# Optimization experiments

Hardware: AMD Instinct MI355X
Metric: run time of the kernel (lower is better)

Reference implementation:

```python
import jax, jax.numpy as jnp
import numpy as np

NUM_EXPERTS = 8
AUX_LOSS_COEF = 0.01


def setup_inputs() -> dict:
    key = jax.random.key(0)
    ks = jax.random.split(key, 5)
    B, S, D, E, H = 4, 2048, 1024, NUM_EXPERTS, 4096
    scale = 0.02  # typical init scale so gelu/softmax stay in sane ranges
    return {
        "hidden_states": jax.random.normal(ks[0], (B, S, D), dtype=jnp.float32),
        "router_w": jax.random.normal(ks[1], (D, E), dtype=jnp.float32) * scale,
        "router_b": jnp.zeros((E,), dtype=jnp.float32),
        "w1": jax.random.normal(ks[2], (E, D, H), dtype=jnp.float32) * scale,
        "b1": jnp.zeros((E, H), dtype=jnp.float32),
        "w2": jax.random.normal(ks[3], (E, H, D), dtype=jnp.float32) * scale,
        "b2": jnp.zeros((E, D), dtype=jnp.float32),
    }


def reference(hidden_states, router_w, router_b, w1, b1, w2, b2):
    B, S, D = hidden_states.shape
    E = w1.shape[0]
    x = hidden_states.reshape(-1, D)  # [T, D] flattened tokens

    # Switch router: top-1 expert, combine weight = softmax prob of chosen expert
    logits = x @ router_w + router_b                      # [T, E]
    probs = jax.nn.softmax(logits, axis=-1)               # [T, E]
    sel = jnp.argmax(logits, axis=-1)                     # [T] int
    gate = jnp.take_along_axis(probs, sel[:, None], axis=1)[:, 0]  # [T]

    # Expert FFNs: per-expert Linear -> gelu -> Linear, masked top-1 combine.
    # Loop is over the small fixed expert count (structurally distinct weights).
    out = jnp.zeros_like(x)
    for e in range(E):
        h = jax.nn.gelu(x @ w1[e] + b1[e])                # [T, H]
        ye = h @ w2[e] + b2[e]                            # [T, D]
        mask = (sel == e).astype(x.dtype)
        out = out + (mask * gate)[:, None] * ye

    # Switch load-balancing auxiliary loss
    mean_probs = probs.mean(axis=0)                       # [E]
    assignments = jnp.mean(jax.nn.one_hot(sel, E, dtype=x.dtype), axis=0)  # [E]
    aux_loss = jnp.sum(mean_probs * assignments) * E
    total_loss = AUX_LOSS_COEF * aux_loss

    return out.reshape(B, S, D), total_loss
```

## Files before the change

### kernel.cpp

```cpp
#include <hip/hip_runtime.h>
#include <cstdint>

typedef __bf16 bf16_t;
typedef __attribute__((ext_vector_type(8))) __bf16 bf16x8;
typedef __attribute__((ext_vector_type(4))) float f32x4;
typedef unsigned short ushort_t;

#define TOKENS 8192
#define DIM 1024
#define HID 4096
#define NEXP 8


__device__ __forceinline__ void gl_lds16(const void* g, void* l) {
  __builtin_amdgcn_global_load_lds(
      (__attribute__((address_space(1))) void*)(void*)g,
      (__attribute__((address_space(3))) void*)l, 16, 0, 0);
}

__device__ __forceinline__ float gelu_fast(float x) {
  float x2 = x * x;
  float z2 = x * (1.59576912f + 0.07135482f * x2);
  float e = __expf(-z2);
  return x * __builtin_amdgcn_rcpf(1.f + e);
}

template <int N>
__device__ __forceinline__ void pwait() {
  __builtin_amdgcn_sched_barrier(0);
  if constexpr (N == 8) asm volatile("s_waitcnt vmcnt(8)" ::: "memory");
  else if constexpr (N == 6) asm volatile("s_waitcnt vmcnt(6)" ::: "memory");
  else asm volatile("s_waitcnt vmcnt(0)" ::: "memory");
  __builtin_amdgcn_sched_barrier(0);
  __builtin_amdgcn_s_barrier();
  __builtin_amdgcn_sched_barrier(0);
}
__device__ __forceinline__ void tbar() {
  __builtin_amdgcn_sched_barrier(0);
  __builtin_amdgcn_s_barrier();
  __builtin_amdgcn_sched_barrier(0);
}

__device__ __forceinline__ int xcd_chunk(int f, int nwg) {
  int q = nwg >> 3, r = nwg & 7;
  int xcd = f & 7, pos = f >> 3;
  return (xcd < r) ? (xcd * (q + 1) + pos) : (r * (q + 1) + (xcd - r) * q + pos);
}

__global__ void router_kernel(const float* __restrict__ x, const float* __restrict__ rw,
                              const float* __restrict__ rbias, bf16_t* __restrict__ xb,
                              int* __restrict__ sel, float* __restrict__ gate,
                              float* __restrict__ pprob, int* __restrict__ pcnt) {
  __shared__ float sprob[NEXP];
  __shared__ int scnt[NEXP];
  int t = threadIdx.x, lane = t & 63, wave = t >> 6;
  if (t < NEXP) { sprob[t] = 0.f; scnt[t] = 0; }
  __syncthreads();
  int tok = blockIdx.x * 4 + wave;
  const float* xp = x + (size_t)tok * DIM + lane * 16;
  float acc[NEXP];
#pragma unroll
  for (int e = 0; e < NEXP; ++e) acc[e] = 0.f;
  ushort_t xv[16];
#pragma unroll
  for (int j = 0; j < 16; j += 4) {
    float4 v = *(const float4*)(xp + j);
    const float* wr = rw + (size_t)(lane * 16 + j) * NEXP;
    float c[4] = {v.x, v.y, v.z, v.w};
#pragma unroll
    for (int d = 0; d < 4; ++d) {
      xv[j + d] = __builtin_bit_cast(ushort_t, (bf16_t)c[d]);
#pragma unroll
      for (int e = 0; e < NEXP; ++e) acc[e] += c[d] * wr[d * NEXP + e];
    }
  }
  {
    uint4* xop = (uint4*)(xb + (size_t)tok * DIM + lane * 16);
    xop[0] = ((uint4*)xv)[0];
    xop[1] = ((uint4*)xv)[1];
  }
#pragma unroll
  for (int s = 1; s < 64; s <<= 1)
#pragma unroll
    for (int e = 0; e < NEXP; ++e) acc[e] += __shfl_xor(acc[e], s);
  if (lane == 0) {
    float lg[NEXP];
#pragma unroll
    for (int e = 0; e < NEXP; ++e) lg[e] = acc[e] + rbias[e];
    float mx = lg[0]; int am = 0;
#pragma unroll
    for (int e = 1; e < NEXP; ++e) if (lg[e] > mx) { mx = lg[e]; am = e; }
    float p[NEXP]; float se = 0.f;
#pragma unroll
    for (int e = 0; e < NEXP; ++e) { p[e] = __expf(lg[e] - mx); se += p[e]; }
    float inv = 1.f / se;
#pragma unroll
    for (int e = 0; e < NEXP; ++e) { p[e] *= inv; atomicAdd(&sprob[e], p[e]); }
    sel[tok] = am;
    gate[tok] = p[am];
    atomicAdd(&scnt[am], 1);
  }
  __syncthreads();
  if (t < NEXP) {
    pprob[blockIdx.x * NEXP + t] = sprob[t];
    pcnt[blockIdx.x * NEXP + t] = scnt[t];
  }
}

__global__ void tcvt2_kernel(const float* __restrict__ w1, const float* __restrict__ w2,
                             bf16_t* __restrict__ w1t, bf16_t* __restrict__ w2t) {
  __shared__ float tile[64][65];
  int y = blockIdx.y;
  int which = y >> 3, e = y & 7;
  int R = which ? HID : DIM;
  int C = which ? DIM : HID;
  const float* src = (which ? w2 : w1) + (size_t)e * R * C;
  bf16_t* dst = (which ? w2t : w1t) + (size_t)e * R * C;
  int cbt = C >> 6;
  int rt = blockIdx.x / cbt, ct = blockIdx.x % cbt;
  int rb = rt * 64, cb = ct * 64;
  int t = threadIdx.x;
  int r = t >> 2, cq = (t & 3) * 16;
  const float* sp = src + (size_t)(rb + r) * C + cb + cq;
#pragma unroll
  for (int j = 0; j < 16; j += 4) {
    float4 v = *(const float4*)(sp + j);
    tile[r][cq + j + 0] = v.x; tile[r][cq + j + 1] = v.y;
    tile[r][cq + j + 2] = v.z; tile[r][cq + j + 3] = v.w;
  }
  __syncthreads();
  int oc = t >> 2, orr = (t & 3) * 16;
  ushort_t tmp[16];
#pragma unroll
  for (int j = 0; j < 16; ++j) {
    bf16_t b = (bf16_t)tile[orr + j][oc];
    tmp[j] = __builtin_bit_cast(ushort_t, b);
  }
  uint4* dp = (uint4*)(dst + (size_t)(cb + oc) * R + rb + orr);
  dp[0] = ((uint4*)tmp)[0];
  dp[1] = ((uint4*)tmp)[1];
}

__global__ void reduce_kernel(const float* __restrict__ pprob, const int* __restrict__ pcnt,
                              int nb, int* __restrict__ meta, float* __restrict__ loss_out) {
  __shared__ float fred[256];
  __shared__ int ired[256];
  int t = threadIdx.x;
  int e = t & 7, i0 = t >> 3;
  float fs = 0.f; int is = 0;
  for (int i = i0; i < nb; i += 32) { fs += pprob[i * 8 + e]; is += pcnt[i * 8 + e]; }
  fred[t] = fs; ired[t] = is;
  __syncthreads();
  if (t < NEXP) {
    float tp = 0.f; int tc = 0;
    for (int j = 0; j < 32; ++j) { tp += fred[j * 8 + t]; tc += ired[j * 8 + t]; }
    meta[t] = tc;
    fred[t] = tp;
    meta[16 + t] = 0;
  }
  __syncthreads();
  if (t == 0) {
    int off = 0; float loss = 0.f; int s1 = 0, s2 = 0;
    for (int q = 0; q < NEXP; ++q) {
      int c = meta[q];
      meta[8 + q] = off;
      int nt1 = (c + 255) >> 8;
      for (int m = 0; m < nt1; ++m) meta[32 + s1++] = (q << 16) | m;
      int nt2 = (c + 127) >> 7;
      for (int m = 0; m < nt2; ++m) meta[96 + s2++] = (q << 16) | m;
      off += c;
      loss += (fred[q] / (float)TOKENS) * ((float)c / (float)TOKENS);
    }
    meta[24] = s1;
    meta[25] = s2;
    *loss_out = loss * (float)NEXP * 0.01f;
  }
}

__global__ void scatter_kernel(const int* __restrict__ sel, int* __restrict__ meta,
                               int* __restrict__ idxl) {
  int tok = blockIdx.x * 256 + threadIdx.x;
  int lane = threadIdx.x & 63;
  int e = sel[tok];
  const int* offsets = meta + 8;
  int* cursors = meta + 16;
#pragma unroll
  for (int ex = 0; ex < NEXP; ++ex) {
    unsigned long long mask = __ballot(e == ex);
    if (e == ex) {
      int leader = __ffsll(mask) - 1;
      int total = __popcll(mask);
      int rank = __popcll(mask & ((1ull << lane) - 1ull));
      int base = 0;
      if (lane == leader) base = atomicAdd(&cursors[ex], total);
      base = __shfl(base, leader);
      idxl[offsets[ex] + base + rank] = tok;
    }
  }
}

#define STG1(Ab, Bb, KT) do {                                              \
    _Pragma("unroll")                                                      \
    for (int c_ = 0; c_ < 4; ++c_) {                                       \
      gl_lds16(ap[c_] + (KT) * 64, Ab + c_ * 4096 + wave * 512);           \
      gl_lds16(bp[c_] + (KT) * 64, Bb + c_ * 4096 + wave * 512);           \
    }                                                                      \
  } while (0)

#define CMP1(Ab, Bb) do {                                                  \
    _Pragma("unroll")                                                      \
    for (int kk = 0; kk < 2; ++kk) {                                       \
      int ks = ((kk * 4 + g) ^ (l15 & 7)) * 8;                             \
      bf16x8 bv[4];                                                        \
      _Pragma("unroll")                                                    \
      for (int n = 0; n < 4; ++n)                                          \
        bv[n] = *(const bf16x8*)&Bb[(wcol * 64 + n * 16 + l15) * 64 + ks]; \
      _Pragma("unroll")                                                    \
      for (int m = 0; m < 8; ++m) {                                        \
        bf16x8 af = *(const bf16x8*)&Ab[(wrow * 128 + m * 16 + l15) * 64 + ks]; \
        _Pragma("unroll")                                                  \
        for (int n = 0; n < 4; ++n)                                        \
          acc[m][n] = __builtin_amdgcn_mfma_f32_16x16x32_bf16(af, bv[n], acc[m][n], 0, 0, 0); \
      }                                                                    \
    }                                                                      \
  } while (0)

__global__ __launch_bounds__(512, 2) void gemm1_kernel(
    const bf16_t* __restrict__ xb, const bf16_t* __restrict__ w1t,
    const float* __restrict__ b1, const int* __restrict__ idxl,
    const int* __restrict__ meta, bf16_t* __restrict__ h) {
  int S = gridDim.x;
  int f = blockIdx.y * S + blockIdx.x;
  int lf = xcd_chunk(f, S * gridDim.y);
  int slot = lf % S, nt = lf / S;
  if (slot >= meta[24]) return;
  int tm = meta[32 + slot];
  int e = tm >> 16, mt = tm & 0xffff;
  int cnt = meta[e];
  int off = meta[8 + e];
  int mBase = mt * 256;
  int nBase = nt * 256;
  __shared__ bf16_t A0[16384], A1[16384], B0[16384], B1[16384];
  int t = threadIdx.x, lane = t & 63, wave = t >> 6;
  int l15 = lane & 15, g = lane >> 4;
  int wrow = wave >> 2, wcol = wave & 3;
  f32x4 acc[8][4];
#pragma unroll
  for (int m = 0; m < 8; ++m)
#pragma unroll
    for (int n = 0; n < 4; ++n) acc[m][n] = (f32x4){0.f, 0.f, 0.f, 0.f};

  int lr3 = lane >> 3;
  int koff = ((lane & 7) ^ lr3) * 8;
  int c1 = cnt - 1;
  const bf16_t* ap[4];
  const bf16_t* bp[4];
  const bf16_t* wb = w1t + (size_t)e * HID * DIM;
#pragma unroll
  for (int c = 0; c < 4; ++c) {
    int r = c * 64 + wave * 8 + lr3;
    int sl = mBase + r; sl = sl < c1 ? sl : c1;
    ap[c] = xb + (size_t)idxl[off + sl] * DIM + koff;
    bp[c] = wb + (size_t)(nBase + r) * DIM + koff;
  }

  STG1(A0, B0, 0);
#pragma unroll 1
  for (int kt = 0; kt < DIM / 64 - 2; kt += 2) {
    STG1(A1, B1, kt + 1); pwait<8>(); CMP1(A0, B0); tbar();
    STG1(A0, B0, kt + 2); pwait<8>(); CMP1(A1, B1); tbar();
  }
  STG1(A1, B1, DIM / 64 - 1); pwait<8>(); CMP1(A0, B0); tbar();
  pwait<0>(); CMP1(A1, B1);

  float bias[4];
#pragma unroll
  for (int n = 0; n < 4; ++n) bias[n] = b1[e * HID + nBase + wcol * 64 + n * 16 + l15];
#pragma unroll
  for (int m = 0; m < 8; ++m) {
    int rb0 = mBase + wrow * 128 + m * 16 + g * 4;
#pragma unroll
    for (int j = 0; j < 4; ++j) {
      int r = rb0 + j;
      if (r < cnt) {
        bf16_t* hp = h + (size_t)(off + r) * HID + nBase + wcol * 64 + l15;
#pragma unroll
        for (int n = 0; n < 4; ++n)
          hp[n * 16] = (bf16_t)gelu_fast(acc[m][n][j] + bias[n]);
      }
    }
  }
}

#define STG2(Ab, Bb, KT) do {                                              \
    _Pragma("unroll")                                                      \
    for (int c_ = 0; c_ < 2; ++c_)                                         \
      gl_lds16(ap[c_] + (KT) * 64, Ab + c_ * 4096 + wave * 512);           \
    _Pragma("unroll")                                                      \
    for (int c_ = 0; c_ < 4; ++c_)                                         \
      gl_lds16(bp[c_] + (KT) * 64, Bb + c_ * 4096 + wave * 512);           \
  } while (0)

#define CMP2(Ab, Bb) do {                                                  \
    _Pragma("unroll")                                                      \
    for (int kk = 0; kk < 2; ++kk) {                                       \
      int ks = ((kk * 4 + g) ^ (l15 & 7)) * 8;                             \
      bf16x8 bv[4];                                                        \
      _Pragma("unroll")                                                    \
      for (int n = 0; n < 4; ++n)                                          \
        bv[n] = *(const bf16x8*)&Bb[(wcol * 64 + n * 16 + l15) * 64 + ks]; \
      _Pragma("unroll")                                                    \
      for (int m = 0; m < 4; ++m) {                                        \
        bf16x8 af = *(const bf16x8*)&Ab[(wrow * 64 + m * 16 + l15) * 64 + ks]; \
        _Pragma("unroll")                                                  \
        for (int n = 0; n < 4; ++n)                                        \
          acc[m][n] = __builtin_amdgcn_mfma_f32_16x16x32_bf16(af, bv[n], acc[m][n], 0, 0, 0); \
      }                                                                    \
    }                                                                      \
  } while (0)

__global__ __launch_bounds__(512, 2) void gemm2_kernel(
    const bf16_t* __restrict__ h, const bf16_t* __restrict__ w2t,
    const float* __restrict__ b2, const int* __restrict__ idxl,
    const float* __restrict__ gate, const int* __restrict__ meta,
    float* __restrict__ out) {
  int S = gridDim.x;
  int f = blockIdx.y * S + blockIdx.x;
  int lf = xcd_chunk(f, S * gridDim.y);
  int slot = lf % S, nt = lf / S;
  if (slot >= meta[25]) return;
  int tm = meta[96 + slot];
  int e = tm >> 16, mt = tm & 0xffff;
  int cnt = meta[e];
  int off = meta[8 + e];
  int mBase = mt * 128;
  int nBase = nt * 256;
  __shared__ bf16_t A0[8192], A1[8192], B0[16384], B1[16384];
  int t = threadIdx.x, lane = t & 63, wave = t >> 6;
  int l15 = lane & 15, g = lane >> 4;
  int wrow = wave >> 2, wcol = wave & 3;
  f32x4 acc[4][4];
#pragma unroll
  for (int m = 0; m < 4; ++m)
#pragma unroll
    for (int n = 0; n < 4; ++n) acc[m][n] = (f32x4){0.f, 0.f, 0.f, 0.f};

  int lr3 = lane >> 3;
  int koff = ((lane & 7) ^ lr3) * 8;
  int c1 = cnt - 1;
  const bf16_t* ap[2];
  const bf16_t* bp[4];
  const bf16_t* wb = w2t + (size_t)e * DIM * HID;
#pragma unroll
  for (int c = 0; c < 2; ++c) {
    int r = c * 64 + wave * 8 + lr3;
    int sl = mBase + r; sl = sl < c1 ? sl : c1;
    ap[c] = h + (size_t)(off + sl) * HID + koff;
  }
#pragma unroll
  for (int c = 0; c < 4; ++c) {
    int r = c * 64 + wave * 8 + lr3;
    bp[c] = wb + (size_t)(nBase + r) * HID + koff;
  }

  STG2(A0, B0, 0);
#pragma unroll 1
  for (int kt = 0; kt < HID / 64 - 2; kt += 2) {
    STG2(A1, B1, kt + 1); pwait<6>(); CMP2(A0, B0); tbar();
    STG2(A0, B0, kt + 2); pwait<6>(); CMP2(A1, B1); tbar();
  }
  STG2(A1, B1, HID / 64 - 1); pwait<6>(); CMP2(A0, B0); tbar();
  pwait<0>(); CMP2(A1, B1);

  float bias[4];
#pragma unroll
  for (int n = 0; n < 4; ++n) bias[n] = b2[e * DIM + nBase + wcol * 64 + n * 16 + l15];
#pragma unroll
  for (int m = 0; m < 4; ++m) {
    int rb0 = mBase + wrow * 64 + m * 16 + g * 4;
#pragma unroll
    for (int j = 0; j < 4; ++j) {
      int r = rb0 + j;
      if (r < cnt) {
        int tok = idxl[off + r];
        float gg = gate[tok];
        float* op = out + (size_t)tok * DIM + nBase + wcol * 64 + l15;
#pragma unroll
        for (int n = 0; n < 4; ++n)
          op[n * 16] = gg * (acc[m][n][j] + bias[n]);
      }
    }
  }
}

extern "C" void kernel_launch(void* const* d_in, const int* in_sizes, int n_in,
                              void* d_out, int out_size, void* d_ws, size_t ws_size,
                              hipStream_t stream) {
  const float* hs = (const float*)d_in[0];
  const float* rw = (const float*)d_in[1];
  const float* rb = (const float*)d_in[2];
  const float* w1 = (const float*)d_in[3];
  const float* b1 = (const float*)d_in[4];
  const float* w2 = (const float*)d_in[5];
  const float* b2 = (const float*)d_in[6];
  float* out = (float*)d_out;
  char* ws = (char*)d_ws;

  bf16_t* xb   = (bf16_t*)(ws + 0);
  bf16_t* w1t  = (bf16_t*)(ws + 16777216);
  bf16_t* w2t  = (bf16_t*)(ws + 83886080);
  bf16_t* hbuf = (bf16_t*)(ws + 150994944);
  int*   sel   = (int*)  (ws + 219152384);
  float* gate  = (float*)(ws + 219185152);
  int*   idxl  = (int*)  (ws + 219217920);
  float* pprob = (float*)(ws + 219250688);
  int*   pcnt  = (int*)  (ws + 219316224);
  int*   meta  = (int*)  (ws + 219381760);

  router_kernel<<<2048, 256, 0, stream>>>(hs, rw, rb, xb, sel, gate, pprob, pcnt);
  tcvt2_kernel<<<dim3(1024, 16), 256, 0, stream>>>(w1, w2, w1t, w2t);
  reduce_kernel<<<1, 256, 0, stream>>>(pprob, pcnt, 2048, meta, out + (out_size - 1));
  scatter_kernel<<<32, 256, 0, stream>>>(sel, meta, idxl);
  gemm1_kernel<<<dim3(40, 16), 512, 0, stream>>>(xb, w1t, b1, idxl, meta, hbuf);
  gemm2_kernel<<<dim3(72, 4), 512, 0, stream>>>(hbuf, w2t, b2, idxl, gate, meta, out);
}
```

Baseline: 440.5 us.

## Switch expert GEMMs to triple-buffered BK=32 pipeline with one barrier per step

Both expert GEMM kernels change from a double-buffered K-tile of 64 to a triple-buffered K-tile of 32 held in a single LDS array. Each stage now issues its loads, computes on an older buffer and then waits, so only one barrier per k-step is needed instead of two. The swizzle is rewritten for the 32-wide rows, MFMA blocks are wrapped in s_setprio, and gemm2's occupancy hint rises to 4 blocks per CU. Intent: deeper load/compute overlap and less sync overhead, at the cost of twice as many k-iterations. The workspace offsets for the small buffers are also shifted.

```diff
diff --git a/kernel.cpp b/kernel.cpp
--- a/kernel.cpp
+++ b/kernel.cpp
@@ -28,14 +28,9 @@
 template <int N>
 __device__ __forceinline__ void pwait() {
   __builtin_amdgcn_sched_barrier(0);
-  if constexpr (N == 8) asm volatile("s_waitcnt vmcnt(8)" ::: "memory");
-  else if constexpr (N == 6) asm volatile("s_waitcnt vmcnt(6)" ::: "memory");
+  if constexpr (N == 4) asm volatile("s_waitcnt vmcnt(4)" ::: "memory");
+  else if constexpr (N == 3) asm volatile("s_waitcnt vmcnt(3)" ::: "memory");
   else asm volatile("s_waitcnt vmcnt(0)" ::: "memory");
-  __builtin_amdgcn_sched_barrier(0);
-  __builtin_amdgcn_s_barrier();
-  __builtin_amdgcn_sched_barrier(0);
-}
-__device__ __forceinline__ void tbar() {
   __builtin_amdgcn_sched_barrier(0);
   __builtin_amdgcn_s_barrier();
   __builtin_amdgcn_sched_barrier(0);
@@ -199,30 +194,30 @@
   }
 }
 
-#define STG1(Ab, Bb, KT) do {                                              \
-    _Pragma("unroll")                                                      \
-    for (int c_ = 0; c_ < 4; ++c_) {                                       \
-      gl_lds16(ap[c_] + (KT) * 64, Ab + c_ * 4096 + wave * 512);           \
-      gl_lds16(bp[c_] + (KT) * 64, Bb + c_ * 4096 + wave * 512);           \
-    }                                                                      \
+#define STG1(Q, KT) do {                                                     \
+    int _kb = (KT) * 32;                                                     \
+    gl_lds16(apA0 + _kb, L1 + (Q) * 16384 + (wave * 16) * 32);               \
+    gl_lds16(apA1 + _kb, L1 + (Q) * 16384 + (128 + wave * 16) * 32);         \
+    gl_lds16(bpB0 + _kb, L1 + (Q) * 16384 + 8192 + (wave * 16) * 32);        \
+    gl_lds16(bpB1 + _kb, L1 + (Q) * 16384 + 8192 + (128 + wave * 16) * 32);  \
   } while (0)
 
-#define CMP1(Ab, Bb) do {                                                  \
-    _Pragma("unroll")                                                      \
-    for (int kk = 0; kk < 2; ++kk) {                                       \
-      int ks = ((kk * 4 + g) ^ (l15 & 7)) * 8;                             \
-      bf16x8 bv[4];                                                        \
-      _Pragma("unroll")                                                    \
-      for (int n = 0; n < 4; ++n)                                          \
-        bv[n] = *(const bf16x8*)&Bb[(wcol * 64 + n * 16 + l15) * 64 + ks]; \
-      _Pragma("unroll")                                                    \
-      for (int m = 0; m < 8; ++m) {                                        \
-        bf16x8 af = *(const bf16x8*)&Ab[(wrow * 128 + m * 16 + l15) * 64 + ks]; \
-        _Pragma("unroll")                                                  \
-        for (int n = 0; n < 4; ++n)                                        \
-          acc[m][n] = __builtin_amdgcn_mfma_f32_16x16x32_bf16(af, bv[n], acc[m][n], 0, 0, 0); \
-      }                                                                    \
-    }                                                                      \
+#define CMP1(Q) do {                                                         \
+    const bf16_t* Ab = L1 + (Q) * 16384;                                     \
+    const bf16_t* Bb = Ab + 8192;                                            \
+    bf16x8 bv[4];                                                            \
+    _Pragma("unroll")                                                        \
+    for (int n = 0; n < 4; ++n)                                              \
+      bv[n] = *(const bf16x8*)&Bb[(wcol * 64 + n * 16 + l15) * 32 + ks];     \
+    __builtin_amdgcn_s_setprio(1);                                           \
+    _Pragma("unroll")                                                        \
+    for (int m = 0; m < 8; ++m) {                                            \
+      bf16x8 af = *(const bf16x8*)&Ab[(wrow * 128 + m * 16 + l15) * 32 + ks];\
+      _Pragma("unroll")                                                      \
+      for (int n = 0; n < 4; ++n)                                            \
+        acc[m][n] = __builtin_amdgcn_mfma_f32_16x16x32_bf16(af, bv[n], acc[m][n], 0, 0, 0); \
+    }                                                                        \
+    __builtin_amdgcn_s_setprio(0);                                           \
   } while (0)
 
 __global__ __launch_bounds__(512, 2) void gemm1_kernel(
@@ -240,38 +235,41 @@
   int off = meta[8 + e];
   int mBase = mt * 256;
   int nBase = nt * 256;
-  __shared__ bf16_t A0[16384], A1[16384], B0[16384], B1[16384];
+  __shared__ bf16_t L1[49152];
   int t = threadIdx.x, lane = t & 63, wave = t >> 6;
   int l15 = lane & 15, g = lane >> 4;
   int wrow = wave >> 2, wcol = wave & 3;
+  int ks = (g ^ (l15 & 3)) * 8;
   f32x4 acc[8][4];
 #pragma unroll
   for (int m = 0; m < 8; ++m)
 #pragma unroll
     for (int n = 0; n < 4; ++n) acc[m][n] = (f32x4){0.f, 0.f, 0.f, 0.f};
 
-  int lr3 = lane >> 3;
-  int koff = ((lane & 7) ^ lr3) * 8;
+  int lr = lane >> 2;
+  int koff = ((lane & 3) ^ (lr & 3)) * 8;
   int c1 = cnt - 1;
-  const bf16_t* ap[4];
-  const bf16_t* bp[4];
+  int r0 = wave * 16 + lr;
+  int s0 = mBase + r0; s0 = s0 < c1 ? s0 : c1;
+  int s1 = mBase + 128 + r0; s1 = s1 < c1 ? s1 : c1;
+  const bf16_t* apA0 = xb + (size_t)idxl[off + s0] * DIM + koff;
+  const bf16_t* apA1 = xb + (size_t)idxl[off + s1] * DIM + koff;
   const bf16_t* wb = w1t + (size_t)e * HID * DIM;
-#pragma unroll
-  for (int c = 0; c < 4; ++c) {
-    int r = c * 64 + wave * 8 + lr3;
-    int sl = mBase + r; sl = sl < c1 ? sl : c1;
-    ap[c] = xb + (size_t)idxl[off + sl] * DIM + koff;
-    bp[c] = wb + (size_t)(nBase + r) * DIM + koff;
-  }
-
-  STG1(A0, B0, 0);
+  const bf16_t* bpB0 = wb + (size_t)(nBase + r0) * DIM + koff;
+  const bf16_t* bpB1 = wb + (size_t)(nBase + 128 + r0) * DIM + koff;
+
+  STG1(0, 0);
+  STG1(1, 1);
+  pwait<4>();
 #pragma unroll 1
-  for (int kt = 0; kt < DIM / 64 - 2; kt += 2) {
-    STG1(A1, B1, kt + 1); pwait<8>(); CMP1(A0, B0); tbar();
-    STG1(A0, B0, kt + 2); pwait<8>(); CMP1(A1, B1); tbar();
-  }
-  STG1(A1, B1, DIM / 64 - 1); pwait<8>(); CMP1(A0, B0); tbar();
-  pwait<0>(); CMP1(A1, B1);
+  for (int kt = 0; kt < 30; kt += 3) {
+    STG1(2, kt + 2); CMP1(0); pwait<4>();
+    STG1(0, kt + 3); CMP1(1); pwait<4>();
+    STG1(1, kt + 4); CMP1(2); pwait<4>();
+  }
+  CMP1(0);
+  pwait<0>();
+  CMP1(1);
 
   float bias[4];
 #pragma unroll
@@ -292,34 +290,32 @@
   }
 }
 
-#define STG2(Ab, Bb, KT) do {                                              \
-    _Pragma("unroll")                                                      \
-    for (int c_ = 0; c_ < 2; ++c_)                                         \
-      gl_lds16(ap[c_] + (KT) * 64, Ab + c_ * 4096 + wave * 512);           \
-    _Pragma("unroll")                                                      \
-    for (int c_ = 0; c_ < 4; ++c_)                                         \
-      gl_lds16(bp[c_] + (KT) * 64, Bb + c_ * 4096 + wave * 512);           \
+#define STG2(Q, KT) do {                                                     \
+    int _kb = (KT) * 32;                                                     \
+    gl_lds16(apA0 + _kb, L2 + (Q) * 12288 + (wave * 16) * 32);               \
+    gl_lds16(bpB0 + _kb, L2 + (Q) * 12288 + 4096 + (wave * 16) * 32);        \
+    gl_lds16(bpB1 + _kb, L2 + (Q) * 12288 + 4096 + (128 + wave * 16) * 32);  \
   } while (0)
 
-#define CMP2(Ab, Bb) do {                                                  \
-    _Pragma("unroll")                                                      \
-    for (int kk = 0; kk < 2; ++kk) {                                       \
-      int ks = ((kk * 4 + g) ^ (l15 & 7)) * 8;                             \
-      bf16x8 bv[4];                                                        \
-      _Pragma("unroll")                                                    \
-      for (int n = 0; n < 4; ++n)                                          \
-        bv[n] = *(const bf16x8*)&Bb[(wcol * 64 + n * 16 + l15) * 64 + ks]; \
-      _Pragma("unroll")                                                    \
-      for (int m = 0; m < 4; ++m) {                                        \
-        bf16x8 af = *(const bf16x8*)&Ab[(wrow * 64 + m * 16 + l15) * 64 + ks]; \
-        _Pragma("unroll")                                                  \
-        for (int n = 0; n < 4; ++n)                                        \
-          acc[m][n] = __builtin_amdgcn_mfma_f32_16x16x32_bf16(af, bv[n], acc[m][n], 0, 0, 0); \
-      }                                                                    \
-    }                                                                      \
+#define CMP2(Q) do {                                                         \
+    const bf16_t* Ab = L2 + (Q) * 12288;                                     \
+    const bf16_t* Bb = Ab + 4096;                                            \
+    bf16x8 bv[4];                                                            \
+    _Pragma("unroll")                                                        \
+    for (int n = 0; n < 4; ++n)                                              \
+      bv[n] = *(const bf16x8*)&Bb[(wcol * 64 + n * 16 + l15) * 32 + ks];     \
+    __builtin_amdgcn_s_setprio(1);                                           \
+    _Pragma("unroll")                                                        \
+    for (int m = 0; m < 4; ++m) {                                            \
+      bf16x8 af = *(const bf16x8*)&Ab[(wrow * 64 + m * 16 + l15) * 32 + ks]; \
+      _Pragma("unroll")                                                      \
+      for (int n = 0; n < 4; ++n)                                            \
+        acc[m][n] = __builtin_amdgcn_mfma_f32_16x16x32_bf16(af, bv[n], acc[m][n], 0, 0, 0); \
+    }                                                                        \
+    __builtin_amdgcn_s_setprio(0);                                           \
   } while (0)
 
-__global__ __launch_bounds__(512, 2) void gemm2_kernel(
+__global__ __launch_bounds__(512, 4) void gemm2_kernel(
     const bf16_t* __restrict__ h, const bf16_t* __restrict__ w2t,
     const float* __restrict__ b2, const int* __restrict__ idxl,
     const float* __restrict__ gate, const int* __restrict__ meta,
@@ -335,42 +331,39 @@
   int off = meta[8 + e];
   int mBase = mt * 128;
   int nBase = nt * 256;
-  __shared__ bf16_t A0[8192], A1[8192], B0[16384], B1[16384];
+  __shared__ bf16_t L2[36864];
   int t = threadIdx.x, lane = t & 63, wave = t >> 6;
   int l15 = lane & 15, g = lane >> 4;
   int wrow = wave >> 2, wcol = wave & 3;
+  int ks = (g ^ (l15 & 3)) * 8;
   f32x4 acc[4][4];
 #pragma unroll
   for (int m = 0; m < 4; ++m)
 #pragma unroll
     for (int n = 0; n < 4; ++n) acc[m][n] = (f32x4){0.f, 0.f, 0.f, 0.f};
 
-  int lr3 = lane >> 3;
-  int koff = ((lane & 7) ^ lr3) * 8;
+  int lr = lane >> 2;
+  int koff = ((lane & 3) ^ (lr & 3)) * 8;
   int c1 = cnt - 1;
-  const bf16_t* ap[2];
-  const bf16_t* bp[4];
+  int r0 = wave * 16 + lr;
+  int s0 = mBase + r0; s0 = s0 < c1 ? s0 : c1;
+  const bf16_t* apA0 = h + (size_t)(off + s0) * HID + koff;
   const bf16_t* wb = w2t + (size_t)e * DIM * HID;
-#pragma unroll
-  for (int c = 0; c < 2; ++c) {
-    int r = c * 64 + wave * 8 + lr3;
-    int sl = mBase + r; sl = sl < c1 ? sl : c1;
-    ap[c] = h + (size_t)(off + sl) * HID + koff;
-  }
-#pragma unroll
-  for (int c = 0; c < 4; ++c) {
-    int r = c * 64 + wave * 8 + lr3;
-    bp[c] = wb + (size_t)(nBase + r) * HID + koff;
-  }
-
-  STG2(A0, B0, 0);
+  const bf16_t* bpB0 = wb + (size_t)(nBase + r0) * HID + koff;
+  const bf16_t* bpB1 = wb + (size_t)(nBase + 128 + r0) * HID + koff;
+
+  STG2(0, 0);
+  STG2(1, 1);
+  pwait<3>();
 #pragma unroll 1
-  for (int kt = 0; kt < HID / 64 - 2; kt += 2) {
-    STG2(A1, B1, kt + 1); pwait<6>(); CMP2(A0, B0); tbar();
-    STG2(A0, B0, kt + 2); pwait<6>(); CMP2(A1, B1); tbar();
-  }
-  STG2(A1, B1, HID / 64 - 1); pwait<6>(); CMP2(A0, B0); tbar();
-  pwait<0>(); CMP2(A1, B1);
+  for (int kt = 0; kt < 126; kt += 3) {
+    STG2(2, kt + 2); CMP2(0); pwait<3>();
+    STG2(0, kt + 3); CMP2(1); pwait<3>();
+    STG2(1, kt + 4); CMP2(2); pwait<3>();
+  }
+  CMP2(0);
+  pwait<0>();
+  CMP2(1);
 
   float bias[4];
 #pragma unroll
@@ -410,12 +403,12 @@
   bf16_t* w1t  = (bf16_t*)(ws + 16777216);
   bf16_t* w2t  = (bf16_t*)(ws + 83886080);
   bf16_t* hbuf = (bf16_t*)(ws + 150994944);
-  int*   sel   = (int*)  (ws + 219152384);
-  float* gate  = (float*)(ws + 219185152);
-  int*   idxl  = (int*)  (ws + 219217920);
-  float* pprob = (float*)(ws + 219250688);
-  int*   pcnt  = (int*)  (ws + 219316224);
-  int*   meta  = (int*)  (ws + 219381760);
+  int*   sel   = (int*)  (ws + 220200960);
+  float* gate  = (float*)(ws + 220233728);
+  int*   idxl  = (int*)  (ws + 220266496);
+  float* pprob = (float*)(ws + 220299264);
+  int*   pcnt  = (int*)  (ws + 220364800);
+  int*   meta  = (int*)  (ws + 220430336);
 
   router_kernel<<<2048, 256, 0, stream>>>(hs, rw, rb, xb, sel, gate, pprob, pcnt);
   tcvt2_kernel<<<dim3(1024, 16), 256, 0, stream>>>(w1, w2, w1t, w2t);
```

After: 396.0 us. 1.11x faster.
